# Kernel tuning notes

Measured on AMD Instinct MI355X. Metric: run time of the kernel, lower is better.

The kernel has to match this reference:

```python
import jax, jax.numpy as jnp
import numpy as np

NUM_EXPERTS = 256
TOP_K = 8
HIDDEN = 7168
N_GROUP = 8
TOPK_GROUP = 4
ROUTED_SCALING_FACTOR = 2.5
NORM_TOPK_PROB = True
TOKENS = 8192


def setup_inputs() -> dict:
    key = jax.random.key(0)
    k1, k2, k3 = jax.random.split(key, 3)
    hidden_states = jax.random.normal(k1, (TOKENS, HIDDEN), dtype=jnp.float32)
    # small init scale keeps router logits in a reasonable sigmoid range
    weight = jax.random.normal(k2, (NUM_EXPERTS, HIDDEN), dtype=jnp.float32) * 0.02
    e_score_correction_bias = jax.random.normal(k3, (NUM_EXPERTS,), dtype=jnp.float32) * 0.01
    return {
        "hidden_states": hidden_states,
        "weight": weight,
        "e_score_correction_bias": e_score_correction_bias,
    }


def reference(hidden_states, weight, e_score_correction_bias):
    hs = hidden_states.reshape(-1, hidden_states.shape[-1]).astype(jnp.float32)
    # [T, E] router logits -> sigmoid scores
    router_logits = hs @ weight.astype(jnp.float32).T
    scores = jax.nn.sigmoid(router_logits)
    scores_for_choice = scores + e_score_correction_bias[None, :]

    experts_per_group = NUM_EXPERTS // N_GROUP
    T = scores_for_choice.shape[0]
    # group score = sum of top-2 biased scores within each group  [T, G]
    grouped = scores_for_choice.reshape(T, N_GROUP, experts_per_group)
    top2_vals, _ = jax.lax.top_k(grouped, 2)
    group_scores = top2_vals.sum(axis=-1)

    # select top groups and build group mask  [T, G]
    _, group_idx = jax.lax.top_k(group_scores, TOPK_GROUP)
    group_mask = jnp.zeros_like(group_scores).at[
        jnp.arange(T)[:, None], group_idx
    ].set(1.0)

    # expand group mask to experts and zero out non-selected groups  [T, E]
    score_mask = jnp.broadcast_to(
        group_mask[:, :, None], (T, N_GROUP, experts_per_group)
    ).reshape(T, NUM_EXPERTS)
    masked_scores = jnp.where(score_mask.astype(bool), scores_for_choice, 0.0)

    # top-k experts over masked biased scores, weights gathered from raw scores
    _, topk_indices = jax.lax.top_k(masked_scores, TOP_K)
    topk_weights = jnp.take_along_axis(scores, topk_indices, axis=1)
    if NORM_TOPK_PROB:
        topk_weights = topk_weights / (
            topk_weights.sum(axis=-1, keepdims=True) + 1e-20
        )
    topk_weights = topk_weights * ROUTED_SCALING_FACTOR
    return topk_indices, topk_weights
```

## Files before the change

### kernel.cpp

```cpp
#include <hip/hip_runtime.h>
#include <float.h>
#include <math.h>

#define TOKENS 8192
#define EXPERTS 256
#define HIDDEN 7168
#define TOPK 8
#define TOPKG 4

#define BM 64
#define BN 256
#define BK 32
#define KSPLIT 8
#define KQ (HIDDEN / KSPLIT)
#define NKTB (KQ / BK)
#define LDR 40

#define TAU_E 6.0e-6f
#define TAU_G 1.2e-5f
#define MAXFB 1024

#define WIMG_ELEMS 1835008

typedef __attribute__((ext_vector_type(8))) short bf16x8;
typedef __attribute__((ext_vector_type(16))) float f32x16;

__device__ inline ushort bf16_rne(float x) {
    uint u = __float_as_uint(x);
    return (ushort)((u + 0x7FFFu + ((u >> 16) & 1u)) >> 16);
}
__device__ inline float bf16_tof(ushort h) { return __uint_as_float((uint)h << 16); }

#define CVTPK(lo, hi) ({ uint r_; asm("v_cvt_pk_bf16_f32 %0, %1, %2" : "=v"(r_) : "v"(lo), "v"(hi)); r_; })
__device__ inline float lo16f(uint u) { return __uint_as_float(u << 16); }
__device__ inline float hi16f(uint u) { return __uint_as_float(u & 0xFFFF0000u); }

#define BAR() do {                                             \
    asm volatile("s_waitcnt lgkmcnt(0)" ::: "memory");         \
    __builtin_amdgcn_s_barrier();                              \
} while (0)

__global__ __launch_bounds__(256) void split_w(const float* __restrict__ W,
                                               ushort* __restrict__ wh,
                                               ushort* __restrict__ wl,
                                               int* __restrict__ cnt) {
    if (blockIdx.x == 0 && threadIdx.x == 0) *cnt = 0;
    const int tau  = blockIdx.x * 256 + threadIdx.x;
    const int j    = tau & 7;
    const int lane = (tau >> 3) & 63;
    const int cg   = (tau >> 9) & 7;
    const int kt16 = tau >> 12;
    const int col  = cg * 32 + (lane & 31);
    const int k    = kt16 * 16 + (lane >> 5) * 8 + j;
    const float w  = W[(size_t)col * HIDDEN + k];
    const ushort h = bf16_rne(w);
    const ushort l = bf16_rne(w - bf16_tof(h));
    wh[tau] = h;
    wl[tau] = l;
}

template <bool ATOMIC>
__global__ __launch_bounds__(512, 4) void logits_mfma(const float* __restrict__ A,
                                                      const ushort* __restrict__ wh,
                                                      const ushort* __restrict__ wl,
                                                      float* __restrict__ dst) {
    __shared__ ushort Ah[2][BM * LDR];
    __shared__ ushort Al[2][BM * LDR];

    const int b  = blockIdx.x;
    const int ks = b & 7;
    const int mb = b >> 3;
    const int row0 = mb * BM;

    const int t = threadIdx.x, lane = t & 63, wn = t >> 6;

    const int sr = t >> 3, q = t & 7;
    const float* Ap = A + (size_t)(row0 + sr) * HIDDEN + (size_t)ks * KQ + q * 4;
    const int sswz = ((sr >> 1) ^ (sr >> 3)) & 3;
    const int sidx = sr * LDR + ((((q >> 1)) ^ sswz) << 3) + (q & 1) * 4;

    int fidx[2][2];
    #pragma unroll
    for (int mi = 0; mi < 2; ++mi) {
        const int r = mi * 32 + (lane & 31);
        const int swz = ((r >> 1) ^ (r >> 3)) & 3;
        #pragma unroll
        for (int kh = 0; kh < 2; ++kh)
            fidx[mi][kh] = r * LDR + (((kh * 2 + (lane >> 5)) ^ swz) << 3);
    }

    const int wlanes = lane * 8;

    f32x16 acc[2];
    acc[0] = (f32x16)0.f;
    acc[1] = (f32x16)0.f;

    float4 aA, aB;
    bf16x8 wAh[2], wAl[2], wBh[2], wBl[2];

    #define WLOAD(DH, DL, KTL) do {                                            \
        const size_t wo = ((size_t)((ks * NKTB + (KTL)) * 2) * 8 + wn) * 512 + wlanes; \
        DH[0] = *(const bf16x8*)(wh + wo);                                     \
        DH[1] = *(const bf16x8*)(wh + wo + 4096);                              \
        DL[0] = *(const bf16x8*)(wl + wo);                                     \
        DL[1] = *(const bf16x8*)(wl + wo + 4096);                              \
    } while (0)

    #define STAGE(BB, R) do {                                                  \
        uint h0 = CVTPK(R.x, R.y), h1 = CVTPK(R.z, R.w);                       \
        float q0 = R.x - lo16f(h0), q1 = R.y - hi16f(h0);                      \
        float q2 = R.z - lo16f(h1), q3 = R.w - hi16f(h1);                      \
        uint l0 = CVTPK(q0, q1), l1 = CVTPK(q2, q3);                           \
        *(uint2*)&Ah[BB][sidx] = make_uint2(h0, h1);                           \
        *(uint2*)&Al[BB][sidx] = make_uint2(l0, l1);                           \
    } while (0)

    #define ALOAD(R, KTL) do {                                                 \
        const int ka = ((KTL) < NKTB ? (KTL) : NKTB - 1) * BK;                 \
        R = *(const float4*)(Ap + ka);                                         \
    } while (0)

    #define MF __builtin_amdgcn_mfma_f32_32x32x16_bf16

    #define ITER(KT, BB, X, WXH, WXL) do {                                     \
                                                        \
        bf16x8 afh0a = *(const bf16x8*)&Ah[BB][fidx[0][0]];                    \
        bf16x8 afh0b = *(const bf16x8*)&Ah[BB][fidx[0][1]];                    \
        bf16x8 afl0a = *(const bf16x8*)&Al[BB][fidx[0][0]];                    \
        bf16x8 afl0b = *(const bf16x8*)&Al[BB][fidx[0][1]];                    \
        STAGE((BB) ^ 1, X);                                                    \
        BAR();                                                                 \
        __builtin_amdgcn_s_setprio(1);                                         \
        acc[0] = MF(afh0a, WXH[0], acc[0], 0, 0, 0);                           \
        acc[0] = MF(afl0a, WXH[0], acc[0], 0, 0, 0);                           \
        acc[0] = MF(afh0a, WXL[0], acc[0], 0, 0, 0);                           \
        acc[0] = MF(afh0b, WXH[1], acc[0], 0, 0, 0);                           \
        acc[0] = MF(afl0b, WXH[1], acc[0], 0, 0, 0);                           \
        acc[0] = MF(afh0b, WXL[1], acc[0], 0, 0, 0);                           \
        __builtin_amdgcn_s_setprio(0);                                         \
                                                        \
        bf16x8 afh1a = *(const bf16x8*)&Ah[BB][fidx[1][0]];                    \
        bf16x8 afh1b = *(const bf16x8*)&Ah[BB][fidx[1][1]];                    \
        bf16x8 afl1a = *(const bf16x8*)&Al[BB][fidx[1][0]];                    \
        bf16x8 afl1b = *(const bf16x8*)&Al[BB][fidx[1][1]];                    \
        ALOAD(X, (KT) + 3);                                                    \
        BAR();                                                                 \
        __builtin_amdgcn_s_setprio(1);                                         \
        acc[1] = MF(afh1a, WXH[0], acc[1], 0, 0, 0);                           \
        acc[1] = MF(afl1a, WXH[0], acc[1], 0, 0, 0);                           \
        acc[1] = MF(afh1a, WXL[0], acc[1], 0, 0, 0);                           \
        acc[1] = MF(afh1b, WXH[1], acc[1], 0, 0, 0);                           \
        acc[1] = MF(afl1b, WXH[1], acc[1], 0, 0, 0);                           \
        acc[1] = MF(afh1b, WXL[1], acc[1], 0, 0, 0);                           \
        __builtin_amdgcn_s_setprio(0);                                         \
        WLOAD(WXH, WXL, ((KT) + 2 < NKTB ? (KT) + 2 : NKTB - 1));              \
    } while (0)

    ALOAD(aA, 0);
    STAGE(0, aA);
    WLOAD(wAh, wAl, 0);
    WLOAD(wBh, wBl, 1);
    ALOAD(aA, 1);
    ALOAD(aB, 2);
    BAR();

    for (int kt2 = 0; kt2 < NKTB; kt2 += 2) {
        ITER(kt2,     0, aA, wAh, wAl);
        ITER(kt2 + 1, 1, aB, wBh, wBl);
    }

    float* o = ATOMIC ? dst : dst + (size_t)ks * TOKENS * EXPERTS;
    #pragma unroll
    for (int mi = 0; mi < 2; ++mi)
        #pragma unroll
        for (int g = 0; g < 16; ++g) {
            const int row = row0 + mi * 32 + (g & 3) + ((g >> 2) << 3) + ((lane >> 5) << 2);
            const int col = wn * 32 + (lane & 31);
            const size_t idx = (size_t)row * EXPERTS + col;
            if (ATOMIC) atomicAdd(o + idx, acc[mi][g]);
            else        o[idx] = acc[mi][g];
        }
    #undef ITER
    #undef MF
    #undef ALOAD
    #undef STAGE
    #undef WLOAD
}

template <int NPART>
__global__ __launch_bounds__(256) void route_margin(const float* __restrict__ p0,
                                                    const float* __restrict__ bias,
                                                    float* __restrict__ out,
                                                    int* __restrict__ cnt,
                                                    int* __restrict__ list) {
    const int lane = threadIdx.x & 63;
    const int t    = blockIdx.x * 4 + (threadIdx.x >> 6);

    float4 lg = *(const float4*)(p0 + (size_t)t * EXPERTS + (lane << 2));
    #pragma unroll
    for (int p = 1; p < NPART; ++p) {
        const float4 l2 = *(const float4*)(p0 + (size_t)p * TOKENS * EXPERTS +
                                           (size_t)t * EXPERTS + (lane << 2));
        lg.x += l2.x; lg.y += l2.y; lg.z += l2.z; lg.w += l2.w;
    }
    const float4 bz = *(const float4*)(bias + (lane << 2));

    const float s0 = 1.f / (1.f + expf(-lg.x));
    const float s1 = 1.f / (1.f + expf(-lg.y));
    const float s2 = 1.f / (1.f + expf(-lg.z));
    const float s3 = 1.f / (1.f + expf(-lg.w));
    const float b0 = s0 + bz.x, b1 = s1 + bz.y, b2 = s2 + bz.z, b3 = s3 + bz.w;

    float hi01 = fmaxf(b0, b1), lo01 = fminf(b0, b1);
    float hi23 = fmaxf(b2, b3), lo23 = fminf(b2, b3);
    float a0v = fmaxf(hi01, hi23);
    float a1v = fmaxf(fminf(hi01, hi23), fmaxf(lo01, lo23));
    #pragma unroll
    for (int off = 1; off < 8; off <<= 1) {
        float o0 = __shfl_xor(a0v, off);
        float o1 = __shfl_xor(a1v, off);
        float n0 = fmaxf(a0v, o0);
        float n1 = fmaxf(fminf(a0v, o0), fmaxf(a1v, o1));
        a0v = n0; a1v = n1;
    }
    const float gscore = a0v + a1v;

    float gsc[8];
    #pragma unroll
    for (int g = 0; g < 8; ++g) gsc[g] = __shfl(gscore, g << 3);

    const int g0 = lane >> 3;
    int myrank = 0;
    float v4 = -1e30f, v5 = -1e30f;
    #pragma unroll
    for (int h = 0; h < 8; ++h) {
        int rk = 0;
        #pragma unroll
        for (int h2 = 0; h2 < 8; ++h2)
            rk += ((gsc[h2] > gsc[h]) || (gsc[h2] == gsc[h] && h2 < h)) ? 1 : 0;
        if (h == g0) myrank = rk;
        if (rk == TOPKG - 1) v4 = gsc[h];
        if (rk == TOPKG)     v5 = gsc[h];
    }
    const bool sel = (myrank < TOPKG);
    const float margin_g = v4 - v5;

    float m0 = sel ? b0 : 0.f;
    float m1 = sel ? b1 : 0.f;
    float m2 = sel ? b2 : 0.f;
    float m3 = sel ? b3 : 0.f;

    float sum = 0.f;
    int myidx = 0; float mysc = 0.f;
    float prev = 0.f, mine = 1e30f;
    #pragma unroll
    for (int rr = 0; rr < TOPK + 1; ++rr) {
        float bv = m0; int bj = 0;
        if (m1 > bv) { bv = m1; bj = 1; }
        if (m2 > bv) { bv = m2; bj = 2; }
        if (m3 > bv) { bv = m3; bj = 3; }
        float bsc = (bj == 0) ? s0 : (bj == 1) ? s1 : (bj == 2) ? s2 : s3;
        int bidx = (lane << 2) | bj;
        #pragma unroll
        for (int off = 1; off < 64; off <<= 1) {
            float ov  = __shfl_xor(bv, off);
            int   oi  = __shfl_xor(bidx, off);
            float osc = __shfl_xor(bsc, off);
            if (ov > bv || (ov == bv && oi < bidx)) { bv = ov; bidx = oi; bsc = osc; }
        }
        if (rr) mine = fminf(mine, prev - bv);
        prev = bv;
        if (rr < TOPK) {
            sum += bsc;
            if (lane == rr) { myidx = bidx; mysc = bsc; }
            if ((bidx >> 2) == lane) {
                const int sl = bidx & 3;
                if      (sl == 0) m0 = -FLT_MAX;
                else if (sl == 1) m1 = -FLT_MAX;
                else if (sl == 2) m2 = -FLT_MAX;
                else              m3 = -FLT_MAX;
            }
        }
    }

    const bool fb = (margin_g < TAU_G) || (mine < TAU_E);
    if (fb) {
        if (lane == 0) { int p = atomicAdd(cnt, 1); if (p < MAXFB) list[p] = t; }
    } else if (lane < TOPK) {
        const size_t base = (size_t)t * TOPK + lane;
        out[base] = (float)myidx;
        out[(size_t)TOKENS * TOPK + base] = mysc / (sum + 1e-20f) * 2.5f;
    }
}

__global__ __launch_bounds__(256) void fallback_logits(const float* __restrict__ A,
                                                       const float* __restrict__ W,
                                                       const int* __restrict__ cnt,
                                                       const int* __restrict__ list,
                                                       double* __restrict__ lgs) {
    const int n = min(*cnt, MAXFB);
    if (n == 0) return;
    __shared__ float Wsh[HIDDEN];
    const int e = blockIdx.x;
    const int tid = threadIdx.x;

    const float4* wg = (const float4*)(W + (size_t)e * HIDDEN);
    for (int i = tid; i < HIDDEN / 4; i += 256)
        ((float4*)Wsh)[i] = wg[i];
    __syncthreads();

    const int lane = tid & 63, wv = tid >> 6;
    for (int ti = wv; ti < n; ti += 4) {
        const int t = list[ti];
        const float* ar = A + (size_t)t * HIDDEN;
        double ac = 0.0;
        #pragma unroll 4
        for (int it = 0; it < HIDDEN / 256; ++it) {
            const int k = it * 256 + (lane << 2);
            const float4 a4 = *(const float4*)(ar + k);
            const float4 w4 = *(const float4*)&Wsh[k];
            ac = fma((double)a4.x, (double)w4.x, ac);
            ac = fma((double)a4.y, (double)w4.y, ac);
            ac = fma((double)a4.z, (double)w4.z, ac);
            ac = fma((double)a4.w, (double)w4.w, ac);
        }
        #pragma unroll
        for (int off = 32; off; off >>= 1)
            ac += __shfl_xor(ac, off);
        if (lane == 0)
            lgs[(size_t)ti * EXPERTS + e] = ac;
    }
}

__global__ __launch_bounds__(256) void fallback_route(const double* __restrict__ lgs,
                                                      const float* __restrict__ bias,
                                                      const int* __restrict__ cnt,
                                                      const int* __restrict__ list,
                                                      float* __restrict__ out) {
    const int n  = min(*cnt, MAXFB);
    const int ti = blockIdx.x * 4 + (threadIdx.x >> 6);
    if (ti >= n) return;
    const int lane = threadIdx.x & 63;
    const int t = list[ti];

    const double l0 = lgs[(size_t)ti * EXPERTS + (lane << 2)];
    const double l1 = lgs[(size_t)ti * EXPERTS + (lane << 2) + 1];
    const double l2 = lgs[(size_t)ti * EXPERTS + (lane << 2) + 2];
    const double l3 = lgs[(size_t)ti * EXPERTS + (lane << 2) + 3];
    const float4 bzf = *(const float4*)(bias + (lane << 2));

    const double s0 = 1.0 / (1.0 + exp(-l0));
    const double s1 = 1.0 / (1.0 + exp(-l1));
    const double s2 = 1.0 / (1.0 + exp(-l2));
    const double s3 = 1.0 / (1.0 + exp(-l3));
    const double b0 = s0 + (double)bzf.x, b1 = s1 + (double)bzf.y;
    const double b2 = s2 + (double)bzf.z, b3 = s3 + (double)bzf.w;

    double hi01 = fmax(b0, b1), lo01 = fmin(b0, b1);
    double hi23 = fmax(b2, b3), lo23 = fmin(b2, b3);
    double a0v = fmax(hi01, hi23);
    double a1v = fmax(fmin(hi01, hi23), fmax(lo01, lo23));
    #pragma unroll
    for (int off = 1; off < 8; off <<= 1) {
        double o0 = __shfl_xor(a0v, off);
        double o1 = __shfl_xor(a1v, off);
        double n0 = fmax(a0v, o0);
        double n1 = fmax(fmin(a0v, o0), fmax(a1v, o1));
        a0v = n0; a1v = n1;
    }
    const double gscore = a0v + a1v;
    double gsc[8];
    #pragma unroll
    for (int g = 0; g < 8; ++g) gsc[g] = __shfl(gscore, g << 3);
    const int g0 = lane >> 3;
    int rank = 0;
    #pragma unroll
    for (int h = 0; h < 8; ++h)
        rank += ((gsc[h] > gscore) || (gsc[h] == gscore && h < g0)) ? 1 : 0;
    const bool sel = (rank < TOPKG);

    double m0 = sel ? b0 : 0.0;
    double m1 = sel ? b1 : 0.0;
    double m2 = sel ? b2 : 0.0;
    double m3 = sel ? b3 : 0.0;

    double sum = 0.0;
    int myidx = 0; double mysc = 0.0;
    #pragma unroll
    for (int rr = 0; rr < TOPK; ++rr) {
        double bv = m0; int bj = 0;
        if (m1 > bv) { bv = m1; bj = 1; }
        if (m2 > bv) { bv = m2; bj = 2; }
        if (m3 > bv) { bv = m3; bj = 3; }
        double bsc = (bj == 0) ? s0 : (bj == 1) ? s1 : (bj == 2) ? s2 : s3;
        int bidx = (lane << 2) | bj;
        #pragma unroll
        for (int off = 1; off < 64; off <<= 1) {
            double ov  = __shfl_xor(bv, off);
            int    oi  = __shfl_xor(bidx, off);
            double osc = __shfl_xor(bsc, off);
            if (ov > bv || (ov == bv && oi < bidx)) { bv = ov; bidx = oi; bsc = osc; }
        }
        sum += bsc;
        if (lane == rr) { myidx = bidx; mysc = bsc; }
        if ((bidx >> 2) == lane) {
            const int sl = bidx & 3;
            if      (sl == 0) m0 = -DBL_MAX;
            else if (sl == 1) m1 = -DBL_MAX;
            else if (sl == 2) m2 = -DBL_MAX;
            else              m3 = -DBL_MAX;
        }
    }
    if (lane < TOPK) {
        const size_t base = (size_t)t * TOPK + lane;
        out[base] = (float)myidx;
        out[(size_t)TOKENS * TOPK + base] = (float)(mysc / (sum + 1e-20) * 2.5);
    }
}

extern "C" void kernel_launch(void* const* d_in, const int* in_sizes, int n_in,
                              void* d_out, int out_size, void* d_ws, size_t ws_size,
                              hipStream_t stream) {
    const float* hs   = (const float*)d_in[0];
    const float* wt   = (const float*)d_in[1];
    const float* bias = (const float*)d_in[2];
    float* out = (float*)d_out;
    char* ws = (char*)d_ws;

    const size_t LGSZ = (size_t)TOKENS * EXPERTS * 4;
    const size_t WIMG = (size_t)WIMG_ELEMS * 2;
    const int NBLK = (TOKENS / BM) * KSPLIT;

    if (ws_size >= KSPLIT * LGSZ + 131072 + 2 * WIMG) {
        float*  part  = (float*)ws;
        int*    cnt   = (int*)(ws + KSPLIT * LGSZ);
        int*    list  = (int*)(ws + KSPLIT * LGSZ + 256);
        ushort* wsh   = (ushort*)(ws + KSPLIT * LGSZ + 131072);
        ushort* wsl   = (ushort*)(ws + KSPLIT * LGSZ + 131072 + WIMG);
        double* lgs64 = (double*)ws;

        split_w<<<WIMG_ELEMS / 256, 256, 0, stream>>>(wt, wsh, wsl, cnt);
        logits_mfma<false><<<NBLK, 512, 0, stream>>>(hs, wsh, wsl, part);
        route_margin<KSPLIT><<<TOKENS / 4, 256, 0, stream>>>(part, bias, out, cnt, list);
        fallback_logits<<<EXPERTS, 256, 0, stream>>>(hs, wt, cnt, list, lgs64);
        fallback_route<<<MAXFB / 4, 256, 0, stream>>>(lgs64, bias, cnt, list, out);
    } else {
        float*  logits = (float*)ws;
        int*    cnt    = (int*)(ws + LGSZ);
        int*    list   = (int*)(ws + LGSZ + 256);
        ushort* wsh    = (ushort*)(ws + LGSZ + 131072);
        ushort* wsl    = (ushort*)(ws + LGSZ + 131072 + WIMG);
        double* lgs64  = (double*)ws;

        hipMemsetAsync(logits, 0, LGSZ, stream);
        split_w<<<WIMG_ELEMS / 256, 256, 0, stream>>>(wt, wsh, wsl, cnt);
        logits_mfma<true><<<NBLK, 512, 0, stream>>>(hs, wsh, wsl, logits);
        route_margin<1><<<TOKENS / 4, 256, 0, stream>>>(logits, bias, out, cnt, list);
        fallback_logits<<<EXPERTS, 256, 0, stream>>>(hs, wt, cnt, list, lgs64);
        fallback_route<<<MAXFB / 4, 256, 0, stream>>>(lgs64, bias, cnt, list, out);
    }
}
```

Measured before the change: 200.4 us.

## Halve K-split and retile waves to 2x4 with one barrier per k-step

Reduces the split-K factor from 8 to 4, so each block covers twice as much of the hidden dimension and fewer partial logit tiles have to be written and reduced. Waves are rearranged into a 2x4 grid in which each wave owns 32 rows by 64 expert columns instead of 64 rows by 32 columns. Each wave therefore reads half as much A data from shared memory per step, and the per-step work needs one barrier instead of two. In exchange, the kernel launches half as many blocks, prefetches W fragments only one step ahead in a single buffer, and host code and the reduction over partials must agree with the new split count.

```diff
diff --git a/kernel.cpp b/kernel.cpp
--- a/kernel.cpp
+++ b/kernel.cpp
@@ -11,7 +11,7 @@
 #define BM 64
 #define BN 256
 #define BK 32
-#define KSPLIT 8
+#define KSPLIT 4
 #define KQ (HIDDEN / KSPLIT)
 #define NKTB (KQ / BK)
 #define LDR 40
@@ -68,25 +68,25 @@
     __shared__ ushort Al[2][BM * LDR];
 
     const int b  = blockIdx.x;
-    const int ks = b & 7;
-    const int mb = b >> 3;
+    const int ks = b & 3;
+    const int mb = b >> 2;
     const int row0 = mb * BM;
 
-    const int t = threadIdx.x, lane = t & 63, wn = t >> 6;
+    const int t = threadIdx.x, lane = t & 63, wid = t >> 6;
+    const int wm = wid >> 2, wn = wid & 3;
 
     const int sr = t >> 3, q = t & 7;
     const float* Ap = A + (size_t)(row0 + sr) * HIDDEN + (size_t)ks * KQ + q * 4;
     const int sswz = ((sr >> 1) ^ (sr >> 3)) & 3;
     const int sidx = sr * LDR + ((((q >> 1)) ^ sswz) << 3) + (q & 1) * 4;
 
-    int fidx[2][2];
-    #pragma unroll
-    for (int mi = 0; mi < 2; ++mi) {
-        const int r = mi * 32 + (lane & 31);
+    int fidx[2];
+    {
+        const int r = wm * 32 + (lane & 31);
         const int swz = ((r >> 1) ^ (r >> 3)) & 3;
         #pragma unroll
         for (int kh = 0; kh < 2; ++kh)
-            fidx[mi][kh] = r * LDR + (((kh * 2 + (lane >> 5)) ^ swz) << 3);
+            fidx[kh] = r * LDR + (((kh * 2 + (lane >> 5)) ^ swz) << 3);
     }
 
     const int wlanes = lane * 8;
@@ -96,14 +96,18 @@
     acc[1] = (f32x16)0.f;
 
     float4 aA, aB;
-    bf16x8 wAh[2], wAl[2], wBh[2], wBl[2];
-
-    #define WLOAD(DH, DL, KTL) do {                                            \
-        const size_t wo = ((size_t)((ks * NKTB + (KTL)) * 2) * 8 + wn) * 512 + wlanes; \
-        DH[0] = *(const bf16x8*)(wh + wo);                                     \
-        DH[1] = *(const bf16x8*)(wh + wo + 4096);                              \
-        DL[0] = *(const bf16x8*)(wl + wo);                                     \
-        DL[1] = *(const bf16x8*)(wl + wo + 4096);                              \
+    bf16x8 wfh[2][2], wfl[2][2];
+
+    #define WLOAD(KTL) do {                                                    \
+        const size_t wo = ((size_t)((ks * NKTB + (KTL)) * 2) * 8 + wn * 2) * 512 + wlanes; \
+        wfh[0][0] = *(const bf16x8*)(wh + wo);                                 \
+        wfh[1][0] = *(const bf16x8*)(wh + wo + 512);                           \
+        wfh[0][1] = *(const bf16x8*)(wh + wo + 4096);                          \
+        wfh[1][1] = *(const bf16x8*)(wh + wo + 4608);                          \
+        wfl[0][0] = *(const bf16x8*)(wl + wo);                                 \
+        wfl[1][0] = *(const bf16x8*)(wl + wo + 512);                           \
+        wfl[0][1] = *(const bf16x8*)(wl + wo + 4096);                          \
+        wfl[1][1] = *(const bf16x8*)(wl + wo + 4608);                          \
     } while (0)
 
     #define STAGE(BB, R) do {                                                  \
@@ -122,63 +126,53 @@
 
     #define MF __builtin_amdgcn_mfma_f32_32x32x16_bf16
 
-    #define ITER(KT, BB, X, WXH, WXL) do {                                     \
-                                                        \
-        bf16x8 afh0a = *(const bf16x8*)&Ah[BB][fidx[0][0]];                    \
-        bf16x8 afh0b = *(const bf16x8*)&Ah[BB][fidx[0][1]];                    \
-        bf16x8 afl0a = *(const bf16x8*)&Al[BB][fidx[0][0]];                    \
-        bf16x8 afl0b = *(const bf16x8*)&Al[BB][fidx[0][1]];                    \
+    #define ITER(KT, BB, X) do {                                               \
+        bf16x8 afh0 = *(const bf16x8*)&Ah[BB][fidx[0]];                        \
+        bf16x8 afh1 = *(const bf16x8*)&Ah[BB][fidx[1]];                        \
+        bf16x8 afl0 = *(const bf16x8*)&Al[BB][fidx[0]];                        \
+        bf16x8 afl1 = *(const bf16x8*)&Al[BB][fidx[1]];                        \
         STAGE((BB) ^ 1, X);                                                    \
-        BAR();                                                                 \
-        __builtin_amdgcn_s_setprio(1);                                         \
-        acc[0] = MF(afh0a, WXH[0], acc[0], 0, 0, 0);                           \
-        acc[0] = MF(afl0a, WXH[0], acc[0], 0, 0, 0);                           \
-        acc[0] = MF(afh0a, WXL[0], acc[0], 0, 0, 0);                           \
-        acc[0] = MF(afh0b, WXH[1], acc[0], 0, 0, 0);                           \
-        acc[0] = MF(afl0b, WXH[1], acc[0], 0, 0, 0);                           \
-        acc[0] = MF(afh0b, WXL[1], acc[0], 0, 0, 0);                           \
-        __builtin_amdgcn_s_setprio(0);                                         \
-                                                        \
-        bf16x8 afh1a = *(const bf16x8*)&Ah[BB][fidx[1][0]];                    \
-        bf16x8 afh1b = *(const bf16x8*)&Ah[BB][fidx[1][1]];                    \
-        bf16x8 afl1a = *(const bf16x8*)&Al[BB][fidx[1][0]];                    \
-        bf16x8 afl1b = *(const bf16x8*)&Al[BB][fidx[1][1]];                    \
         ALOAD(X, (KT) + 3);                                                    \
         BAR();                                                                 \
         __builtin_amdgcn_s_setprio(1);                                         \
-        acc[1] = MF(afh1a, WXH[0], acc[1], 0, 0, 0);                           \
-        acc[1] = MF(afl1a, WXH[0], acc[1], 0, 0, 0);                           \
-        acc[1] = MF(afh1a, WXL[0], acc[1], 0, 0, 0);                           \
-        acc[1] = MF(afh1b, WXH[1], acc[1], 0, 0, 0);                           \
-        acc[1] = MF(afl1b, WXH[1], acc[1], 0, 0, 0);                           \
-        acc[1] = MF(afh1b, WXL[1], acc[1], 0, 0, 0);                           \
+        acc[0] = MF(afh0, wfh[0][0], acc[0], 0, 0, 0);                         \
+        acc[0] = MF(afl0, wfh[0][0], acc[0], 0, 0, 0);                         \
+        acc[0] = MF(afh0, wfl[0][0], acc[0], 0, 0, 0);                         \
+        acc[1] = MF(afh0, wfh[1][0], acc[1], 0, 0, 0);                         \
+        acc[1] = MF(afl0, wfh[1][0], acc[1], 0, 0, 0);                         \
+        acc[1] = MF(afh0, wfl[1][0], acc[1], 0, 0, 0);                         \
+        acc[0] = MF(afh1, wfh[0][1], acc[0], 0, 0, 0);                         \
+        acc[0] = MF(afl1, wfh[0][1], acc[0], 0, 0, 0);                         \
+        acc[0] = MF(afh1, wfl[0][1], acc[0], 0, 0, 0);                         \
+        acc[1] = MF(afh1, wfh[1][1], acc[1], 0, 0, 0);                         \
+        acc[1] = MF(afl1, wfh[1][1], acc[1], 0, 0, 0);                         \
+        acc[1] = MF(afh1, wfl[1][1], acc[1], 0, 0, 0);                         \
         __builtin_amdgcn_s_setprio(0);                                         \
-        WLOAD(WXH, WXL, ((KT) + 2 < NKTB ? (KT) + 2 : NKTB - 1));              \
+        WLOAD(((KT) + 1 < NKTB ? (KT) + 1 : NKTB - 1));                        \
     } while (0)
 
     ALOAD(aA, 0);
     STAGE(0, aA);
-    WLOAD(wAh, wAl, 0);
-    WLOAD(wBh, wBl, 1);
+    WLOAD(0);
     ALOAD(aA, 1);
     ALOAD(aB, 2);
     BAR();
 
     for (int kt2 = 0; kt2 < NKTB; kt2 += 2) {
-        ITER(kt2,     0, aA, wAh, wAl);
-        ITER(kt2 + 1, 1, aB, wBh, wBl);
+        ITER(kt2,     0, aA);
+        ITER(kt2 + 1, 1, aB);
     }
 
     float* o = ATOMIC ? dst : dst + (size_t)ks * TOKENS * EXPERTS;
     #pragma unroll
-    for (int mi = 0; mi < 2; ++mi)
+    for (int n = 0; n < 2; ++n)
         #pragma unroll
         for (int g = 0; g < 16; ++g) {
-            const int row = row0 + mi * 32 + (g & 3) + ((g >> 2) << 3) + ((lane >> 5) << 2);
-            const int col = wn * 32 + (lane & 31);
+            const int row = row0 + wm * 32 + (g & 3) + ((g >> 2) << 3) + ((lane >> 5) << 2);
+            const int col = wn * 64 + n * 32 + (lane & 31);
             const size_t idx = (size_t)row * EXPERTS + col;
-            if (ATOMIC) atomicAdd(o + idx, acc[mi][g]);
-            else        o[idx] = acc[mi][g];
+            if (ATOMIC) atomicAdd(o + idx, acc[n][g]);
+            else        o[idx] = acc[n][g];
         }
     #undef ITER
     #undef MF
```

Measured after the change: 212.3 us. 6.0% more time.
